# Kernel optimization log

Hardware: AMD Instinct MI355X
Metric: run time of the kernel (lower is better)

Reference implementation:

```python
import jax, jax.numpy as jnp
import numpy as np

LAM = 0.5
MU = 0.1
RHO = 0.05


def setup_inputs() -> dict:
    key = jax.random.key(0)
    k1, k2, k3 = jax.random.split(key, 3)
    B, C, S = 65536, 10, 128
    predictions = jax.random.normal(k1, (B, C), dtype=jnp.float32)
    targets = jax.random.randint(k2, (B,), 0, C)
    noise = jax.random.normal(k3, (S, B, C), dtype=jnp.float32)
    return {"predictions": predictions, "targets": targets, "noise": noise}


def reference(predictions, targets, noise):
    B, C = predictions.shape
    # log-softmax of predictions, reused for all cross-entropies
    logp = jax.nn.log_softmax(predictions, axis=1)  # [B, C]
    # wstar = CE(predictions, hard targets), mean over batch
    wstar = -jnp.mean(jnp.take_along_axis(logp, targets[:, None], axis=1))
    one_hot = jax.nn.one_hot(targets, C, dtype=predictions.dtype)  # [B, C]
    # soft targets for each of the n_samples noise draws (vectorized over s)
    soft_lam = jax.nn.softmax(LAM * noise + one_hot, axis=-1)  # [S, B, C]
    soft = jax.nn.softmax(noise + one_hot, axis=-1)            # [S, B, C]
    # CE with soft (probability) targets: -mean_b sum_c target * log_softmax(pred)
    w = -jnp.einsum('sbc,bc->s', soft, logp) / B       # [S]
    wt = -jnp.einsum('sbc,bc->s', soft_lam, logp) / B  # [S]
    noise2 = jnp.sum(noise * noise, axis=(1, 2))       # [S]
    sc1 = jnp.maximum(wstar - wt, 0.0)
    sc2 = jnp.maximum(wstar - w + MU * noise2 / 2, 0.0)
    sc3 = jnp.maximum(wt - (1.0 - LAM) * wstar + LAM * w
                      + MU * LAM * (1.0 - LAM) * noise2 / 2, 0.0)
    sc = jnp.sum(sc1 + sc2 + sc3)  # aggregation='sum'
    return wstar + RHO * sc
```

## Files before the change

### kernel.cpp

```cpp
#include <hip/hip_runtime.h>

#define LAM 0.5f
#define MU 0.1f
#define RHO 0.05f
#define CLS 10
#define ROWS 256
#define SG 16
#define L2E  1.4426950408889634f
#define HL2E 0.7213475204444817f
#define EINV 0.36787944117144233f

typedef const __attribute__((address_space(1))) char gchar;
typedef __attribute__((address_space(3))) char lchar;

__device__ __forceinline__ float waveReduceSum(float v) {
#pragma unroll
    for (int m = 1; m < 64; m <<= 1) v += __shfl_xor(v, m, 64);
    return v;
}

__device__ __forceinline__ float waveSumDPP(float v) {
#define DPP_ADD(CTRL)                                                          \
    v += __int_as_float(__builtin_amdgcn_update_dpp(                           \
        0, __float_as_int(v), (CTRL), 0xf, 0xf, true));
    DPP_ADD(0x111)
    DPP_ADD(0x112)
    DPP_ADD(0x114)
    DPP_ADD(0x118)
    DPP_ADD(0x142)
    DPP_ADD(0x143)
#undef DPP_ADD
    return __int_as_float(__builtin_amdgcn_readlane(__float_as_int(v), 63));
}

__device__ __forceinline__ void dmaTile(const float4* srcBase, float* dstBase,
                                        int wid, int lane) {
    const float4* s = srcBase + wid * 160;
    float* d = dstBase + wid * 640;
    __builtin_amdgcn_global_load_lds((gchar*)(const char*)(s + lane),
                                     (lchar*)(char*)d, 16, 0, 0);
    __builtin_amdgcn_global_load_lds((gchar*)(const char*)(s + 64 + lane),
                                     (lchar*)(char*)(d + 256), 16, 0, 0);
    if (lane < 32)
        __builtin_amdgcn_global_load_lds((gchar*)(const char*)(s + 128 + lane),
                                         (lchar*)(char*)(d + 512), 16, 0, 0);
}

__global__ __launch_bounds__(256) void main_kernel(
    const float* __restrict__ noise, const float* __restrict__ pred,
    const int* __restrict__ tgt,
    float* __restrict__ wstarPart, float* __restrict__ partials, int B) {
    __shared__ float buf0[ROWS * CLS];
    __shared__ float buf1[ROWS * CLS];

    const int tid = threadIdx.x;
    const int lane = tid & 63, wid = tid >> 6;
    const int nChunks = B / ROWS;
    const int chunk = (int)blockIdx.x % nChunks;
    const int sg = (int)blockIdx.x / nChunks;
    const int rowBase = chunk * ROWS;
    const int s0 = sg * SG;
    const int nPart = nChunks * 4;

    const int t = tgt[rowBase + tid];
    __builtin_amdgcn_sched_barrier(0);

    const size_t sStride4 = (size_t)B * CLS / 4;
    const float4* noiseT = (const float4*)(noise + (size_t)rowBase * CLS)
                           + (size_t)s0 * sStride4;

    dmaTile((const float4*)(pred + (size_t)rowBase * CLS), buf0, wid, lane);
    dmaTile(noiseT, buf1, wid, lane);
    asm volatile("s_waitcnt vmcnt(3)" ::: "memory");
    __builtin_amdgcn_sched_barrier(0);

    float x[CLS];
    {
        const float2* r2 = (const float2*)(buf0 + tid * CLS);
#pragma unroll
        for (int j = 0; j < 5; j++) { float2 v = r2[j]; x[2*j] = v.x; x[2*j+1] = v.y; }
    }
    float mx = x[0];
#pragma unroll
    for (int c = 1; c < CLS; c++) mx = fmaxf(mx, x[c]);
    float z = 0.f;
#pragma unroll
    for (int c = 0; c < CLS; c++) z += __expf(x[c] - mx);
    float lse = mx + __logf(z);

    float lp[CLS], lpk[CLS], kk[CLS], bias[CLS];
    float xt = 0.f;
#pragma unroll
    for (int c = 0; c < CLS; c++) {
        bool e = (c == t);
        float lpv = x[c] - lse;
        lp[c] = lpv;
        kk[c] = e ? EINV : 1.f;
        lpk[c] = lpv * kk[c];
        bias[c] = e ? L2E : 0.f;
        xt += e ? x[c] : 0.f;
    }
    float keep;
    {
        float rce = waveSumDPP(lse - xt);
        keep = (lane == 48) ? rce : 0.f;
    }

    const float4* srcNext = noiseT + sStride4;

#define BODY(CUR, NXT, SI)                                                     \
    {                                                                          \
        const int si = (SI);                                                   \
        if (si < SG - 1) {                                                     \
            dmaTile(srcNext, (NXT), wid, lane);                                \
            srcNext += sStride4;                                               \
            asm volatile("s_waitcnt vmcnt(3)" ::: "memory");                   \
        } else {                                                               \
            asm volatile("s_waitcnt vmcnt(0)" ::: "memory");                   \
        }                                                                      \
        __builtin_amdgcn_sched_barrier(0);                                     \
        float nn[CLS];                                                         \
        {                                                                      \
            const float2* r2 = (const float2*)((CUR) + tid * CLS);             \
            _Pragma("unroll")                                                  \
            for (int j = 0; j < 5; j++) {                                      \
                float2 v = r2[j]; nn[2*j] = v.x; nn[2*j+1] = v.y;              \
            }                                                                  \
        }                                                                      \
        float Z = 0.f, Zl = 0.f, dot = 0.f, dotl = 0.f, sq = 0.f;              \
        _Pragma("unroll")                                                      \
        for (int c = 0; c < CLS; c++) {                                        \
            float a  = fmaf(nn[c], HL2E, bias[c]);                             \
            float pl = exp2f(a);                                               \
            float t1 = pl * pl;                                                \
            Zl += pl;                                                          \
            dotl = fmaf(pl, lp[c], dotl);                                      \
            Z    = fmaf(t1, kk[c], Z);                                         \
            dot  = fmaf(t1, lpk[c], dot);                                      \
            sq   = fmaf(nn[c], nn[c], sq);                                     \
        }                                                                      \
        float rw  = waveSumDPP(__fdividef(dot, Z));                            \
        float rwt = waveSumDPP(__fdividef(dotl, Zl));                          \
        float rn2 = waveSumDPP(sq);                                            \
        keep = (lane == si * 3    ) ? rw  : keep;                              \
        keep = (lane == si * 3 + 1) ? rwt : keep;                              \
        keep = (lane == si * 3 + 2) ? rn2 : keep;                              \
    }

    for (int sb = 0; sb < SG; sb += 2) {
        BODY(buf1, buf0, sb);
        BODY(buf0, buf1, sb + 1);
    }
#undef BODY

    if (lane < SG * 3) {
        int si = lane / 3, k = lane - 3 * si;
        partials[(size_t)((s0 + si) * 3 + k) * nPart + chunk * 4 + wid] = keep;
    }
    if (sg == 0 && lane == 48)
        wstarPart[chunk * 4 + wid] = keep;
}

__global__ __launch_bounds__(256) void reduce_kernel(
    const float* __restrict__ partials, const float* __restrict__ wstarPart,
    float* __restrict__ scPart, float* __restrict__ wsum, int B, int nPart) {
    __shared__ float red[4][4];
    const int s = blockIdx.x, tid = threadIdx.x;
    const int lane = tid & 63, wid = tid >> 6;
    const float* p = partials + (size_t)s * 3 * nPart;
    float a = 0.f, b = 0.f, c = 0.f, wv = 0.f;
    for (int j = tid; j < nPart; j += 256) {
        a  += p[j];
        b  += p[nPart + j];
        c  += p[2 * nPart + j];
        wv += wstarPart[j];
    }
    a = waveReduceSum(a); b = waveReduceSum(b);
    c = waveReduceSum(c); wv = waveReduceSum(wv);
    if (lane == 0) { red[wid][0] = a; red[wid][1] = b; red[wid][2] = c; red[wid][3] = wv; }
    __syncthreads();
    if (tid == 0) {
        float ra = red[0][0] + red[1][0] + red[2][0] + red[3][0];
        float rb = red[0][1] + red[1][1] + red[2][1] + red[3][1];
        float rc = red[0][2] + red[1][2] + red[2][2] + red[3][2];
        float rw = red[0][3] + red[1][3] + red[2][3] + red[3][3];
        float invB = 1.0f / (float)B;
        float wstar = rw * invB;
        float w  = -ra * invB;
        float wt = -rb * invB;
        float n2 =  rc;
        float sc1 = fmaxf(wstar - wt, 0.f);
        float sc2 = fmaxf(wstar - w + MU * n2 * 0.5f, 0.f);
        float sc3 = fmaxf(wt - (1.f - LAM) * wstar + LAM * w
                          + MU * LAM * (1.f - LAM) * n2 * 0.5f, 0.f);
        scPart[s] = sc1 + sc2 + sc3;
        if (s == 0) wsum[0] = rw;
    }
}

__global__ __launch_bounds__(256) void finalize_kernel(
    const float* __restrict__ scPart, const float* __restrict__ wsum,
    float* __restrict__ out, int B, int S) {
    __shared__ float red[2];
    const int tid = threadIdx.x, lane = tid & 63, wid = tid >> 6;
    float v = (tid < S) ? scPart[tid] : 0.f;
    if (tid < 128) {
        float r = waveReduceSum(v);
        if (lane == 0) red[wid] = r;
    }
    __syncthreads();
    if (tid == 0)
        out[0] = wsum[0] / (float)B + RHO * (red[0] + red[1]);
}

extern "C" void kernel_launch(void* const* d_in, const int* in_sizes, int n_in,
                              void* d_out, int out_size, void* d_ws, size_t ws_size,
                              hipStream_t stream) {
    const float* pred  = (const float*)d_in[0];
    const int*   tgt   = (const int*)d_in[1];
    const float* noise = (const float*)d_in[2];
    float* out = (float*)d_out;

    int B = in_sizes[1];
    int S = in_sizes[2] / in_sizes[0];
    int nChunks = B / ROWS;
    int nSG = S / SG;
    int nPart = nChunks * 4;

    float* ws = (float*)d_ws;
    float* wstarPart = ws;
    float* scPart    = ws + 1024;
    float* wsum      = ws + 1152;
    float* partials  = ws + 2048;

    main_kernel<<<nSG * nChunks, 256, 0, stream>>>(noise, pred, tgt,
                                                   wstarPart, partials, B);
    reduce_kernel<<<S, 256, 0, stream>>>(partials, wstarPart, scPart, wsum,
                                         B, nPart);
    finalize_kernel<<<1, 256, 0, stream>>>(scPart, wsum, out, B, S);
}
```

Measured before the change: 75.07 us.

## Triple-buffer noise tiles and double samples per block

Each block now processes 32 noise samples instead of 16, which halves the grid and the number of times predictions and log-softmax are recomputed. The LDS staging moves from double to triple buffering, so two tiles are in flight while the current one is consumed, and the loop is fully unrolled with modulo-3 buffer indexing. Per-sample results are packed into two lane-indexed registers. The cost is more LDS per block, which may reduce occupancy, fewer blocks for latency hiding, and a larger unrolled body.

```diff
diff --git a/kernel.cpp b/kernel.cpp
--- a/kernel.cpp
+++ b/kernel.cpp
@@ -5,7 +5,7 @@
 #define RHO 0.05f
 #define CLS 10
 #define ROWS 256
-#define SG 16
+#define SG 32
 #define L2E  1.4426950408889634f
 #define HL2E 0.7213475204444817f
 #define EINV 0.36787944117144233f
@@ -50,9 +50,7 @@
     const float* __restrict__ noise, const float* __restrict__ pred,
     const int* __restrict__ tgt,
     float* __restrict__ wstarPart, float* __restrict__ partials, int B) {
-    __shared__ float buf0[ROWS * CLS];
-    __shared__ float buf1[ROWS * CLS];
-
+    __shared__ float bufb[3 * ROWS * CLS / 1 * 1];
     const int tid = threadIdx.x;
     const int lane = tid & 63, wid = tid >> 6;
     const int nChunks = B / ROWS;
@@ -69,14 +67,15 @@
     const float4* noiseT = (const float4*)(noise + (size_t)rowBase * CLS)
                            + (size_t)s0 * sStride4;
 
-    dmaTile((const float4*)(pred + (size_t)rowBase * CLS), buf0, wid, lane);
-    dmaTile(noiseT, buf1, wid, lane);
-    asm volatile("s_waitcnt vmcnt(3)" ::: "memory");
+    dmaTile((const float4*)(pred + (size_t)rowBase * CLS), bufb + 2 * 2560, wid, lane);
+    dmaTile(noiseT,            bufb,        wid, lane);
+    dmaTile(noiseT + sStride4, bufb + 2560, wid, lane);
+    asm volatile("s_waitcnt vmcnt(6)" ::: "memory");
     __builtin_amdgcn_sched_barrier(0);
 
     float x[CLS];
     {
-        const float2* r2 = (const float2*)(buf0 + tid * CLS);
+        const float2* r2 = (const float2*)(bufb + 2 * 2560 + tid * CLS);
 #pragma unroll
         for (int j = 0; j < 5; j++) { float2 v = r2[j]; x[2*j] = v.x; x[2*j+1] = v.y; }
     }
@@ -100,65 +99,70 @@
         bias[c] = e ? L2E : 0.f;
         xt += e ? x[c] : 0.f;
     }
-    float keep;
+    float keepW;
     {
         float rce = waveSumDPP(lse - xt);
-        keep = (lane == 48) ? rce : 0.f;
-    }
-
-    const float4* srcNext = noiseT + sStride4;
-
-#define BODY(CUR, NXT, SI)                                                     \
-    {                                                                          \
-        const int si = (SI);                                                   \
-        if (si < SG - 1) {                                                     \
-            dmaTile(srcNext, (NXT), wid, lane);                                \
-            srcNext += sStride4;                                               \
-            asm volatile("s_waitcnt vmcnt(3)" ::: "memory");                   \
-        } else {                                                               \
-            asm volatile("s_waitcnt vmcnt(0)" ::: "memory");                   \
-        }                                                                      \
-        __builtin_amdgcn_sched_barrier(0);                                     \
-        float nn[CLS];                                                         \
-        {                                                                      \
-            const float2* r2 = (const float2*)((CUR) + tid * CLS);             \
-            _Pragma("unroll")                                                  \
-            for (int j = 0; j < 5; j++) {                                      \
-                float2 v = r2[j]; nn[2*j] = v.x; nn[2*j+1] = v.y;              \
-            }                                                                  \
-        }                                                                      \
-        float Z = 0.f, Zl = 0.f, dot = 0.f, dotl = 0.f, sq = 0.f;              \
-        _Pragma("unroll")                                                      \
-        for (int c = 0; c < CLS; c++) {                                        \
-            float a  = fmaf(nn[c], HL2E, bias[c]);                             \
-            float pl = exp2f(a);                                               \
-            float t1 = pl * pl;                                                \
-            Zl += pl;                                                          \
-            dotl = fmaf(pl, lp[c], dotl);                                      \
-            Z    = fmaf(t1, kk[c], Z);                                         \
-            dot  = fmaf(t1, lpk[c], dot);                                      \
-            sq   = fmaf(nn[c], nn[c], sq);                                     \
-        }                                                                      \
-        float rw  = waveSumDPP(__fdividef(dot, Z));                            \
-        float rwt = waveSumDPP(__fdividef(dotl, Zl));                          \
-        float rn2 = waveSumDPP(sq);                                            \
-        keep = (lane == si * 3    ) ? rw  : keep;                              \
-        keep = (lane == si * 3 + 1) ? rwt : keep;                              \
-        keep = (lane == si * 3 + 2) ? rn2 : keep;                              \
-    }
-
-    for (int sb = 0; sb < SG; sb += 2) {
-        BODY(buf1, buf0, sb);
-        BODY(buf0, buf1, sb + 1);
-    }
-#undef BODY
-
-    if (lane < SG * 3) {
+        keepW = (lane == 48) ? rce : 0.f;
+    }
+
+    float keepX = 0.f, keepY = 0.f;
+    const float4* srcNext = noiseT + 2 * sStride4;
+
+#pragma unroll
+    for (int it = 0; it < SG; ++it) {
+        const float* CUR = bufb + (it % 3) * 2560;
+        if (it < SG - 2) {
+            dmaTile(srcNext, bufb + ((it + 2) % 3) * 2560, wid, lane);
+            srcNext += sStride4;
+            asm volatile("s_waitcnt vmcnt(6)" ::: "memory");
+        } else if (it == SG - 2) {
+            asm volatile("s_waitcnt vmcnt(3)" ::: "memory");
+        } else {
+            asm volatile("s_waitcnt vmcnt(0)" ::: "memory");
+        }
+        __builtin_amdgcn_sched_barrier(0);
+
+        float nn[CLS];
+        {
+            const float2* r2 = (const float2*)(CUR + tid * CLS);
+#pragma unroll
+            for (int j = 0; j < 5; j++) { float2 v = r2[j]; nn[2*j] = v.x; nn[2*j+1] = v.y; }
+        }
+        float Z = 0.f, Zl = 0.f, dot = 0.f, dotl = 0.f, sq = 0.f;
+#pragma unroll
+        for (int c = 0; c < CLS; c++) {
+            float a  = fmaf(nn[c], HL2E, bias[c]);
+            float pl = exp2f(a);
+            float t1 = pl * pl;
+            Zl += pl;
+            dotl = fmaf(pl, lp[c], dotl);
+            Z    = fmaf(t1, kk[c], Z);
+            dot  = fmaf(t1, lpk[c], dot);
+            sq   = fmaf(nn[c], nn[c], sq);
+        }
+        float rw  = waveSumDPP(__fdividef(dot, Z));
+        float rwt = waveSumDPP(__fdividef(dotl, Zl));
+        float rn2 = waveSumDPP(sq);
+        if (it < 16) {
+            keepX = (lane == it * 3    ) ? rw  : keepX;
+            keepX = (lane == it * 3 + 1) ? rwt : keepX;
+            keepX = (lane == it * 3 + 2) ? rn2 : keepX;
+        } else {
+            const int j = it - 16;
+            keepY = (lane == j * 3    ) ? rw  : keepY;
+            keepY = (lane == j * 3 + 1) ? rwt : keepY;
+            keepY = (lane == j * 3 + 2) ? rn2 : keepY;
+        }
+    }
+
+    if (lane < 48) {
         int si = lane / 3, k = lane - 3 * si;
-        partials[(size_t)((s0 + si) * 3 + k) * nPart + chunk * 4 + wid] = keep;
+        size_t col = (size_t)chunk * 4 + wid;
+        partials[(size_t)((s0 + si) * 3 + k) * nPart + col] = keepX;
+        partials[(size_t)((s0 + 16 + si) * 3 + k) * nPart + col] = keepY;
     }
     if (sg == 0 && lane == 48)
-        wstarPart[chunk * 4 + wid] = keep;
+        wstarPart[chunk * 4 + wid] = keepW;
 }
 
 __global__ __launch_bounds__(256) void reduce_kernel(
```

New measurement: 73.80 us. Within noise of the previous version (-1.7%).
